# Kernel optimization log

Hardware: AMD Instinct MI355X
Metric: run time of the kernel (lower is better)

## Reference

```python
import jax, jax.numpy as jnp
import numpy as np

B, NT, K = 2048, 8192, 128   # traces, time samples, spline knots
DT = 1e-3


def setup_inputs() -> dict:
    key = jax.random.key(0)
    k1, k2, k3 = jax.random.split(key, 3)
    t = jnp.arange(NT, dtype=jnp.float32) * DT                       # uniform grid
    f = jax.random.uniform(k1, (B, NT), dtype=jnp.float32) + 0.1     # positive densities
    # normalize each trace to unit trapezoid mass so the CDF F lies in [0, 1]
    mass = (0.5 * (f[:, :1] + f[:, -1:]) + f[:, 1:-1].sum(-1, keepdims=True)) * DT
    f = f / mass
    # per-trace monotone knot grids on [0, 1] (spline breakpoints of the quantile fn)
    interior = jnp.sort(jax.random.uniform(k2, (B, K - 2), dtype=jnp.float32), axis=-1)
    knots = jnp.concatenate(
        [jnp.zeros((B, 1), jnp.float32), interior, jnp.full((B, 1), 1.0 + 1e-6, jnp.float32)],
        axis=-1,
    )
    # piecewise-cubic coefficients (a, b, c, d) per interval
    coeffs = 0.1 * jax.random.normal(k3, (B, K - 1, 4), dtype=jnp.float32)
    return {"f": f, "t": t, "knots": knots, "coeffs": coeffs}


def _cum_trap(f, dt):
    # cumulative trapezoid along last dim, zero-prepended (preserve_dims=True)
    inc = 0.5 * (f[..., 1:] + f[..., :-1]) * dt
    u = jnp.cumsum(inc, axis=-1)
    zero = jnp.zeros(u.shape[:-1] + (1,), u.dtype)
    return jnp.concatenate([zero, u], axis=-1)


def _spline_eval(knots, coeffs, q):
    # knots: [K], coeffs: [K-1, 4], q: [nt] -> [nt]
    idx = jnp.clip(jnp.searchsorted(knots, q, side="right") - 1, 0, knots.shape[0] - 2)
    dx = q - knots[idx]
    c = coeffs[idx]  # [nt, 4]
    return c[..., 0] + dx * (c[..., 1] + dx * (c[..., 2] + dx * c[..., 3]))


def reference(f, t, knots, coeffs):
    dt = t[1] - t[0]
    F = _cum_trap(f, dt)                               # [B, NT] CDF
    off_diag = jax.vmap(_spline_eval)(knots, coeffs, F)  # batched spline lookup
    g = (t - off_diag) ** 2 * f                        # broadcast t over batch
    # trapezoid reduction with uniform dx
    return (0.5 * (g[..., 0] + g[..., -1]) + g[..., 1:-1].sum(-1)) * dt
```

## Files before the change

kernel.cpp:

```cpp
#include <hip/hip_runtime.h>


#define NT 8192
#define K 128
#define NTHREADS 1024
#define ELEMS (NT / NTHREADS)
#define NWAVES (NTHREADS / 64)
#define LUTG 256

__global__ __launch_bounds__(NTHREADS, 8) void w2loss_kernel(
    const float* __restrict__ f,
    const float* __restrict__ t,
    const float* __restrict__ knots,
    const float* __restrict__ coeffs,
    float* __restrict__ out)
{
    const int b    = blockIdx.x;
    const int tid  = threadIdx.x;
    const int lane = tid & 63;
    const int wave = tid >> 6;

    __shared__ float  s_knots[K];
    __shared__ float4 s_coeffs[K - 1];
    __shared__ int    s_lut[LUTG];
    __shared__ float  s_wsum[NWAVES];
    __shared__ float  s_wred[NWAVES];
    __shared__ float  s_f0;

    if (tid < K) s_knots[tid] = knots[(size_t)b * K + tid];
    if (tid < K - 1)
        s_coeffs[tid] =
            reinterpret_cast<const float4*>(coeffs + (size_t)b * (K - 1) * 4)[tid];

    const float4* fb4 =
        reinterpret_cast<const float4*>(f + (size_t)b * NT + tid * ELEMS);
    float fv[ELEMS];
#pragma unroll
    for (int i = 0; i < ELEMS / 4; ++i) {
        float4 v = fb4[i];
        fv[4 * i + 0] = v.x; fv[4 * i + 1] = v.y;
        fv[4 * i + 2] = v.z; fv[4 * i + 3] = v.w;
    }

    float local = 0.f;
#pragma unroll
    for (int i = 0; i < ELEMS; ++i) local += fv[i];

    float scan = local;
#pragma unroll
    for (int d = 1; d < 64; d <<= 1) {
        float up = __shfl_up(scan, d, 64);
        if (lane >= d) scan += up;
    }
    if (lane == 63) s_wsum[wave] = scan;
    if (tid == 0)  s_f0 = fv[0];
    __syncthreads();

    if (tid < LUTG) {
        float gval = (float)tid * (1.0f / (float)LUTG);
        int p = 0;
#pragma unroll
        for (int step = 64; step >= 1; step >>= 1) {
            int np = p + step;
            if (np <= K - 1 && s_knots[np] <= gval) p = np;
        }
        s_lut[tid] = p;
    }
    __syncthreads();

    float waveoff = 0.f;
    for (int w = 0; w < wave; ++w) waveoff += s_wsum[w];

    const float f0      = s_f0;
    const float dt      = t[1] - t[0];
    const float half_dt = 0.5f * dt;

    const float S_incl_first = waveoff + (scan - local) + fv[0];
    float F = (S_incl_first - 0.5f * (f0 + fv[0])) * dt;

    const int   base = tid * ELEMS;
    const float tb   = (float)base * dt;

    int g   = (int)(F * (float)LUTG);
    g       = g > (LUTG - 1) ? (LUTG - 1) : (g < 0 ? 0 : g);
    int idx = s_lut[g];
    while (idx < K - 2 && s_knots[idx + 1] <= F) ++idx;
    float  kn_lo = s_knots[idx];
    float  kn_hi = s_knots[idx + 1];
    float4 c     = s_coeffs[idx];

    float acc, term_first, term_last = 0.f;
    {
        float dx = F - kn_lo;
        float sp = c.x + dx * (c.y + dx * (c.z + dx * c.w));
        float d0 = tb - sp;
        term_first = d0 * d0 * fv[0];
        acc = term_first;
    }

#pragma unroll
    for (int i = 1; i < ELEMS; ++i) {
        F = fmaf(fv[i - 1] + fv[i], half_dt, F);
        if (kn_hi <= F && idx < K - 2) {
            do { ++idx; kn_hi = s_knots[idx + 1]; } while (kn_hi <= F && idx < K - 2);
            kn_lo = s_knots[idx];
            c     = s_coeffs[idx];
        }
        float dx = F - kn_lo;
        float sp = c.x + dx * (c.y + dx * (c.z + dx * c.w));
        float tt = fmaf((float)i, dt, tb);
        float d  = tt - sp;
        float term = d * d * fv[i];
        acc += term;
        if (i == ELEMS - 1) term_last = term;
    }

    if (base == 0)          acc -= 0.5f * term_first;
    if (base + ELEMS == NT) acc -= 0.5f * term_last;

#pragma unroll
    for (int d = 32; d >= 1; d >>= 1) acc += __shfl_down(acc, d, 64);
    if (lane == 0) s_wred[wave] = acc;
    __syncthreads();
    if (tid == 0) {
        float r = 0.f;
#pragma unroll
        for (int w = 0; w < NWAVES; ++w) r += s_wred[w];
        out[b] = r * dt;
    }
}

extern "C" void kernel_launch(void* const* d_in, const int* in_sizes, int n_in,
                              void* d_out, int out_size, void* d_ws, size_t ws_size,
                              hipStream_t stream) {
    const float* f      = (const float*)d_in[0];
    const float* t      = (const float*)d_in[1];
    const float* knots  = (const float*)d_in[2];
    const float* coeffs = (const float*)d_in[3];
    float* out          = (float*)d_out;

    const int Btr = in_sizes[0] / NT;
    w2loss_kernel<<<Btr, NTHREADS, 0, stream>>>(f, t, knots, coeffs, out);
}
```

Before: 106.4 us.

## Halve block size, shuffle-scan wave offsets, and prefetch next spline interval

Halves the block to 512 threads, so each thread handles 16 samples instead of 8, and lowers the launch-bounds occupancy hint to match. The serial loop over earlier waves' sums is replaced by a wave-level shuffle prefix scan. The spline lookup now keeps coefficients for both the current and the next interval and picks one with a select. A divergent shared-memory reload is then only needed when the CDF skips past two knots. The trade-offs are longer per-thread serial chains, higher register pressure, and fewer threads to hide latency.

```diff
diff --git a/kernel.cpp b/kernel.cpp
--- a/kernel.cpp
+++ b/kernel.cpp
@@ -3,12 +3,12 @@
 
 #define NT 8192
 #define K 128
-#define NTHREADS 1024
+#define NTHREADS 512
 #define ELEMS (NT / NTHREADS)
 #define NWAVES (NTHREADS / 64)
 #define LUTG 256
 
-__global__ __launch_bounds__(NTHREADS, 8) void w2loss_kernel(
+__global__ __launch_bounds__(NTHREADS, 4) void w2loss_kernel(
     const float* __restrict__ f,
     const float* __restrict__ t,
     const float* __restrict__ knots,
@@ -68,8 +68,13 @@
     }
     __syncthreads();
 
-    float waveoff = 0.f;
-    for (int w = 0; w < wave; ++w) waveoff += s_wsum[w];
+    float wv = (lane < NWAVES) ? s_wsum[lane] : 0.f;
+#pragma unroll
+    for (int d = 1; d < NWAVES; d <<= 1) {
+        float up = __shfl_up(wv, d, 64);
+        if (lane >= d) wv += up;
+    }
+    const float waveoff = (wave == 0) ? 0.f : __shfl(wv, wave - 1, 64);
 
     const float f0      = s_f0;
     const float dt      = t[1] - t[0];
@@ -81,18 +86,21 @@
     const int   base = tid * ELEMS;
     const float tb   = (float)base * dt;
 
-    int g   = (int)(F * (float)LUTG);
-    g       = g > (LUTG - 1) ? (LUTG - 1) : (g < 0 ? 0 : g);
-    int idx = s_lut[g];
-    while (idx < K - 2 && s_knots[idx + 1] <= F) ++idx;
-    float  kn_lo = s_knots[idx];
-    float  kn_hi = s_knots[idx + 1];
-    float4 c     = s_coeffs[idx];
+    int g  = (int)(F * (float)LUTG);
+    g      = g > (LUTG - 1) ? (LUTG - 1) : (g < 0 ? 0 : g);
+    int i0 = s_lut[g];
+    while (i0 < K - 2 && s_knots[i0 + 1] <= F) ++i0;
+    float  kn0_lo = s_knots[i0];
+    float  kn0_hi = s_knots[i0 + 1];
+    float4 c0     = s_coeffs[i0];
+    int    j1     = (i0 < K - 2) ? i0 + 1 : K - 2;
+    float4 c1     = s_coeffs[j1];
+    float  kn1_hi = (i0 + 2 <= K - 1) ? s_knots[i0 + 2] : 3.4e38f;
 
     float acc, term_first, term_last = 0.f;
     {
-        float dx = F - kn_lo;
-        float sp = c.x + dx * (c.y + dx * (c.z + dx * c.w));
+        float dx = F - kn0_lo;
+        float sp = c0.x + dx * (c0.y + dx * (c0.z + dx * c0.w));
         float d0 = tb - sp;
         term_first = d0 * d0 * fv[0];
         acc = term_first;
@@ -101,13 +109,28 @@
 #pragma unroll
     for (int i = 1; i < ELEMS; ++i) {
         F = fmaf(fv[i - 1] + fv[i], half_dt, F);
-        if (kn_hi <= F && idx < K - 2) {
-            do { ++idx; kn_hi = s_knots[idx + 1]; } while (kn_hi <= F && idx < K - 2);
-            kn_lo = s_knots[idx];
-            c     = s_coeffs[idx];
+
+        if (kn1_hi <= F) {
+            int idx = i0 + 2;
+            while (idx < K - 2 && s_knots[idx + 1] <= F) ++idx;
+            i0     = idx;
+            kn0_lo = s_knots[i0];
+            kn0_hi = s_knots[i0 + 1];
+            c0     = s_coeffs[i0];
+            j1     = (i0 < K - 2) ? i0 + 1 : K - 2;
+            c1     = s_coeffs[j1];
+            kn1_hi = (i0 + 2 <= K - 1) ? s_knots[i0 + 2] : 3.4e38f;
         }
-        float dx = F - kn_lo;
-        float sp = c.x + dx * (c.y + dx * (c.z + dx * c.w));
+
+        bool  use1 = (kn0_hi <= F);
+        float klo  = use1 ? kn0_hi : kn0_lo;
+        float cx   = use1 ? c1.x : c0.x;
+        float cy   = use1 ? c1.y : c0.y;
+        float cz   = use1 ? c1.z : c0.z;
+        float cw   = use1 ? c1.w : c0.w;
+
+        float dx = F - klo;
+        float sp = cx + dx * (cy + dx * (cz + dx * cw));
         float tt = fmaf((float)i, dt, tb);
         float d  = tt - sp;
         float term = d * d * fv[i];
```

Result: slower. 221.1 us (+107.7%).
